# Performance work log

Measured on AMD Instinct MI355X. Metric: run time of the kernel, lower is better.

## Reference

```python
import jax, jax.numpy as jnp
import numpy as np

NEG_INF = -9e15
ALPHA = 0.2  # LeakyReLU negative slope used by GraphAttentionLayer


def gat_layer(h, adj, W, a, concat):
    # h: [N, din], W: [din, dout], a: [2*dout, 1]
    Wh = h @ W                              # [N, dout]
    dout = W.shape[1]
    f1 = Wh @ a[:dout]                      # [N, 1]
    f2 = Wh @ a[dout:]                      # [N, 1]
    e = jax.nn.leaky_relu(f1 + f2.T, negative_slope=ALPHA)   # [N, N]
    att = jax.nn.softmax(jnp.where(adj > 0, e, NEG_INF), axis=1)
    hp = att @ Wh                           # [N, dout]
    out = jax.nn.elu(hp) if concat else hp
    return out, att


def setup_inputs() -> dict:
    key = jax.random.key(0)
    ks = jax.random.split(key, 6)
    N, d_in, d_hid, d_out = 8192, 256, 128, 64
    features = jax.random.normal(ks[0], (N, d_in), dtype=jnp.float32)
    adj = (jax.random.uniform(ks[1], (N, N)) < 0.01).astype(jnp.float32)
    s = 0.1
    W1 = jax.random.normal(ks[2], (d_in, d_hid), dtype=jnp.float32) * s
    a1 = jax.random.normal(ks[3], (2 * d_hid, 1), dtype=jnp.float32) * s
    W2 = jax.random.normal(ks[4], (d_hid, d_out), dtype=jnp.float32) * s
    a2 = jax.random.normal(ks[5], (2 * d_out, 1), dtype=jnp.float32) * s
    return {"features": features, "adj": adj, "W1": W1, "a1": a1, "W2": W2, "a2": a2}


def reference(features, adj, W1, a1, W2, a2):
    h1, attention = gat_layer(features, adj, W1, a1, concat=True)   # gat1 (elu)
    h2, _ = gat_layer(h1, adj, W2, a2, concat=False)                 # gat2
    row_mask = (adj.sum(axis=1) > 0).astype(h2.dtype)[:, None]       # [N, 1]
    genenet_res = jax.nn.sigmoid(h2 @ h2.T) * row_mask               # inner-product decoder
    return h2, genenet_res, attention
```

## Files before the change

kernel.cpp:

```cpp
#include <hip/hip_runtime.h>
#include <cstdint>
#include <cstddef>

#define NN 8192
#define DIN 256
#define DHID 128
#define DOUT 64
#define MAXDEG 256

using short8  = __attribute__((ext_vector_type(8))) short;
using floatx4 = __attribute__((ext_vector_type(4))) float;

__device__ inline unsigned short f2bf(float x) {
  union { float f; unsigned u; } c; c.f = x;
  unsigned r = (c.u + 0x7FFFu + ((c.u >> 16) & 1u)) >> 16;
  return (unsigned short)r;
}

__global__ __launch_bounds__(256) void k_gemm1(const float* __restrict__ feat,
                                               const float* __restrict__ W1,
                                               float* __restrict__ Wh1) {
  __shared__ float Ws[64 * DHID];
  __shared__ float Fs[64][65];
  const int tid = threadIdx.x;
  const int cx = tid & 31;
  const int ry = tid >> 5;
  const int r0 = blockIdx.x * 64;
  float acc[8][4] = {};
  for (int kc = 0; kc < DIN; kc += 64) {
    const float4* src = (const float4*)(W1 + (size_t)kc * DHID);
    float4* dst = (float4*)Ws;
    #pragma unroll
    for (int i = 0; i < 8; ++i) dst[i * 256 + tid] = src[i * 256 + tid];
    #pragma unroll
    for (int i = 0; i < 4; ++i) {
      int idx = i * 256 + tid;
      int row = idx >> 4, kq = idx & 15;
      float4 v = *(const float4*)(feat + (size_t)(r0 + row) * DIN + kc + kq * 4);
      Fs[row][kq * 4 + 0] = v.x; Fs[row][kq * 4 + 1] = v.y;
      Fs[row][kq * 4 + 2] = v.z; Fs[row][kq * 4 + 3] = v.w;
    }
    __syncthreads();
    #pragma unroll 4
    for (int k = 0; k < 64; ++k) {
      float4 w = *(const float4*)(Ws + k * DHID + cx * 4);
      #pragma unroll
      for (int r = 0; r < 8; ++r) {
        float f = Fs[ry * 8 + r][k];
        acc[r][0] += f * w.x; acc[r][1] += f * w.y;
        acc[r][2] += f * w.z; acc[r][3] += f * w.w;
      }
    }
    __syncthreads();
  }
  #pragma unroll
  for (int r = 0; r < 8; ++r) {
    float4 o = make_float4(acc[r][0], acc[r][1], acc[r][2], acc[r][3]);
    *(float4*)(Wh1 + (size_t)(r0 + ry * 8 + r) * DHID + cx * 4) = o;
  }
}

__global__ __launch_bounds__(256) void k_gemm2(const float* __restrict__ h1,
                                               const float* __restrict__ W2,
                                               float* __restrict__ Wh2) {
  __shared__ float Ws[64 * DOUT];
  __shared__ float Fs[128][65];
  const int tid = threadIdx.x;
  const int cx = tid & 15;
  const int ry = tid >> 4;
  const int r0 = blockIdx.x * 128;
  float acc[8][4] = {};
  for (int kc = 0; kc < DHID; kc += 64) {
    const float4* src = (const float4*)(W2 + (size_t)kc * DOUT);
    float4* dst = (float4*)Ws;
    #pragma unroll
    for (int i = 0; i < 4; ++i) dst[i * 256 + tid] = src[i * 256 + tid];
    #pragma unroll
    for (int i = 0; i < 8; ++i) {
      int idx = i * 256 + tid;
      int row = idx >> 4, kq = idx & 15;
      float4 v = *(const float4*)(h1 + (size_t)(r0 + row) * DHID + kc + kq * 4);
      Fs[row][kq * 4 + 0] = v.x; Fs[row][kq * 4 + 1] = v.y;
      Fs[row][kq * 4 + 2] = v.z; Fs[row][kq * 4 + 3] = v.w;
    }
    __syncthreads();
    #pragma unroll 4
    for (int k = 0; k < 64; ++k) {
      float4 w = *(const float4*)(Ws + k * DOUT + cx * 4);
      #pragma unroll
      for (int r = 0; r < 8; ++r) {
        float f = Fs[ry * 8 + r][k];
        acc[r][0] += f * w.x; acc[r][1] += f * w.y;
        acc[r][2] += f * w.z; acc[r][3] += f * w.w;
      }
    }
    __syncthreads();
  }
  #pragma unroll
  for (int r = 0; r < 8; ++r) {
    float4 o = make_float4(acc[r][0], acc[r][1], acc[r][2], acc[r][3]);
    *(float4*)(Wh2 + (size_t)(r0 + ry * 8 + r) * DOUT + cx * 4) = o;
  }
}

__global__ __launch_bounds__(256) void k_fvec1(const float* __restrict__ Wh1,
                                               const float* __restrict__ a1,
                                               float* __restrict__ f1, float* __restrict__ f2) {
  int wv = threadIdx.x >> 6, lane = threadIdx.x & 63;
  int row = blockIdx.x * 4 + wv;
  float2 x = *(const float2*)(Wh1 + (size_t)row * DHID + lane * 2);
  float2 u = *(const float2*)(a1 + lane * 2);
  float2 v = *(const float2*)(a1 + DHID + lane * 2);
  float s1 = x.x * u.x + x.y * u.y;
  float s2 = x.x * v.x + x.y * v.y;
  #pragma unroll
  for (int off = 32; off; off >>= 1) { s1 += __shfl_down(s1, off); s2 += __shfl_down(s2, off); }
  if (lane == 0) { f1[row] = s1; f2[row] = s2; }
}

__global__ __launch_bounds__(256) void k_fvec2(const float* __restrict__ Wh2,
                                               const float* __restrict__ a2,
                                               float* __restrict__ f1, float* __restrict__ f2) {
  int wv = threadIdx.x >> 6, lane = threadIdx.x & 63;
  int row = blockIdx.x * 4 + wv;
  float x = Wh2[(size_t)row * DOUT + lane];
  float s1 = x * a2[lane];
  float s2 = x * a2[DOUT + lane];
  #pragma unroll
  for (int off = 32; off; off >>= 1) { s1 += __shfl_down(s1, off); s2 += __shfl_down(s2, off); }
  if (lane == 0) { f1[row] = s1; f2[row] = s2; }
}

__global__ __launch_bounds__(256) void k_att1(const float* __restrict__ adj,
                                              const float* __restrict__ f1,
                                              const float* __restrict__ f2,
                                              const float* __restrict__ Wh1,
                                              float* __restrict__ att_out,
                                              float* __restrict__ h1,
                                              int* __restrict__ csr,
                                              int* __restrict__ degree) {
  __shared__ int   scols[MAXDEG];
  __shared__ float sval[MAXDEG];
  __shared__ float red[256];
  __shared__ int   cnt;
  const int tid = threadIdx.x;
  const int row = blockIdx.x;
  if (tid == 0) cnt = 0;
  __syncthreads();
  const float4* arow = (const float4*)(adj + (size_t)row * NN);
  #pragma unroll
  for (int it = 0; it < 8; ++it) {
    int idx = it * 256 + tid;
    float4 v = arow[idx];
    if (v.x > 0.0f) { int s = atomicAdd(&cnt, 1); if (s < MAXDEG) scols[s] = idx * 4 + 0; }
    if (v.y > 0.0f) { int s = atomicAdd(&cnt, 1); if (s < MAXDEG) scols[s] = idx * 4 + 1; }
    if (v.z > 0.0f) { int s = atomicAdd(&cnt, 1); if (s < MAXDEG) scols[s] = idx * 4 + 2; }
    if (v.w > 0.0f) { int s = atomicAdd(&cnt, 1); if (s < MAXDEG) scols[s] = idx * 4 + 3; }
  }
  __syncthreads();
  const int deg = min(cnt, MAXDEG);
  if (tid == 0) degree[row] = deg;
  for (int t = tid; t < deg; t += 256) csr[(size_t)row * MAXDEG + t] = scols[t];
  const float base = f1[row];
  float lmax = -3.0e38f;
  for (int t = tid; t < deg; t += 256) {
    float e = base + f2[scols[t]];
    e = e > 0.0f ? e : 0.2f * e;
    sval[t] = e;
    lmax = fmaxf(lmax, e);
  }
  red[tid] = lmax; __syncthreads();
  #pragma unroll
  for (int off = 128; off; off >>= 1) { if (tid < off) red[tid] = fmaxf(red[tid], red[tid + off]); __syncthreads(); }
  const float m = red[0];
  __syncthreads();
  float lsum = 0.0f;
  for (int t = tid; t < deg; t += 256) { float ex = expf(sval[t] - m); sval[t] = ex; lsum += ex; }
  red[tid] = lsum; __syncthreads();
  #pragma unroll
  for (int off = 128; off; off >>= 1) { if (tid < off) red[tid] += red[tid + off]; __syncthreads(); }
  const float inv = 1.0f / red[0];
  __syncthreads();
  for (int t = tid; t < deg; t += 256) sval[t] *= inv;
  const float fill = (deg == 0) ? (1.0f / (float)NN) : 0.0f;
  float4 fv = make_float4(fill, fill, fill, fill);
  float4* orow = (float4*)(att_out + (size_t)row * NN);
  #pragma unroll
  for (int it = 0; it < 8; ++it) orow[it * 256 + tid] = fv;
  __syncthreads();
  for (int t = tid; t < deg; t += 256) att_out[(size_t)row * NN + scols[t]] = sval[t];
  const int d = tid & 127, g = tid >> 7;
  float acc = 0.0f;
  if (deg > 0) {
    for (int t = g; t < deg; t += 2) acc += sval[t] * Wh1[(size_t)scols[t] * DHID + d];
  } else {
    for (int r = g; r < NN; r += 2) acc += Wh1[(size_t)r * DHID + d];
    acc *= (1.0f / (float)NN);
  }
  __syncthreads();
  red[tid] = acc; __syncthreads();
  if (tid < 128) {
    float h = red[tid] + red[tid + 128];
    h = h > 0.0f ? h : (expf(h) - 1.0f);
    h1[(size_t)row * DHID + tid] = h;
  }
}

__global__ __launch_bounds__(256) void k_att2(const int* __restrict__ csr,
                                              const int* __restrict__ degree,
                                              const float* __restrict__ f1,
                                              const float* __restrict__ f2,
                                              const float* __restrict__ Wh2,
                                              float* __restrict__ h2) {
  __shared__ int   scols[MAXDEG];
  __shared__ float sval[MAXDEG];
  __shared__ float red[256];
  const int tid = threadIdx.x;
  const int row = blockIdx.x;
  const int deg = degree[row];
  for (int t = tid; t < deg; t += 256) scols[t] = csr[(size_t)row * MAXDEG + t];
  __syncthreads();
  const float base = f1[row];
  float lmax = -3.0e38f;
  for (int t = tid; t < deg; t += 256) {
    float e = base + f2[scols[t]];
    e = e > 0.0f ? e : 0.2f * e;
    sval[t] = e;
    lmax = fmaxf(lmax, e);
  }
  red[tid] = lmax; __syncthreads();
  #pragma unroll
  for (int off = 128; off; off >>= 1) { if (tid < off) red[tid] = fmaxf(red[tid], red[tid + off]); __syncthreads(); }
  const float m = red[0];
  __syncthreads();
  float lsum = 0.0f;
  for (int t = tid; t < deg; t += 256) { float ex = expf(sval[t] - m); sval[t] = ex; lsum += ex; }
  red[tid] = lsum; __syncthreads();
  #pragma unroll
  for (int off = 128; off; off >>= 1) { if (tid < off) red[tid] += red[tid + off]; __syncthreads(); }
  const float inv = 1.0f / red[0];
  __syncthreads();
  for (int t = tid; t < deg; t += 256) sval[t] *= inv;
  __syncthreads();
  const int d = tid & 63, g = tid >> 6;
  float acc = 0.0f;
  if (deg > 0) {
    for (int t = g; t < deg; t += 4) acc += sval[t] * Wh2[(size_t)scols[t] * DOUT + d];
  } else {
    for (int r = g; r < NN; r += 4) acc += Wh2[(size_t)r * DOUT + d];
    acc *= (1.0f / (float)NN);
  }
  red[tid] = acc; __syncthreads();
  if (tid < 64) h2[(size_t)row * DOUT + tid] = red[tid] + red[tid + 64] + red[tid + 128] + red[tid + 192];
}

__global__ __launch_bounds__(256) void k_genenet(const float* __restrict__ h2,
                                                 const int* __restrict__ degree,
                                                 float* __restrict__ out) {
  __shared__ unsigned short As[128 * 72];
  __shared__ unsigned short Bs[128 * 72];
  __shared__ float dmask[128];
  const int tid = threadIdx.x;
  const int R0 = blockIdx.x * 128, C0 = blockIdx.y * 128;
  #pragma unroll
  for (int it = 0; it < 8; ++it) {
    int idx = it * 256 + tid;
    int r = idx >> 4, kq = idx & 15;
    float4 va = *(const float4*)(h2 + (size_t)(R0 + r) * DOUT + kq * 4);
    float4 vb = *(const float4*)(h2 + (size_t)(C0 + r) * DOUT + kq * 4);
    ushort4 ba, bb;
    ba.x = f2bf(va.x); ba.y = f2bf(va.y); ba.z = f2bf(va.z); ba.w = f2bf(va.w);
    bb.x = f2bf(vb.x); bb.y = f2bf(vb.y); bb.z = f2bf(vb.z); bb.w = f2bf(vb.w);
    *(ushort4*)&As[r * 72 + kq * 4] = ba;
    *(ushort4*)&Bs[r * 72 + kq * 4] = bb;
  }
  if (tid < 128) dmask[tid] = (degree[R0 + tid] > 0) ? 1.0f : 0.0f;
  __syncthreads();
  const int wave = tid >> 6, lane = tid & 63;
  const int wr = wave >> 1, wc = wave & 1;
  const int lr = lane & 15, quad = lane >> 4;
  short8 a[4][2], b[4][2];
  #pragma unroll
  for (int mi = 0; mi < 4; ++mi) {
    int r = wr * 64 + mi * 16 + lr;
    a[mi][0] = *(const short8*)(const void*)&As[r * 72 + quad * 8];
    a[mi][1] = *(const short8*)(const void*)&As[r * 72 + quad * 8 + 32];
  }
  #pragma unroll
  for (int ni = 0; ni < 4; ++ni) {
    int r = wc * 64 + ni * 16 + lr;
    b[ni][0] = *(const short8*)(const void*)&Bs[r * 72 + quad * 8];
    b[ni][1] = *(const short8*)(const void*)&Bs[r * 72 + quad * 8 + 32];
  }
  floatx4 acc[4][4] = {};
  #pragma unroll
  for (int mi = 0; mi < 4; ++mi)
    #pragma unroll
    for (int ni = 0; ni < 4; ++ni) {
      acc[mi][ni] = __builtin_amdgcn_mfma_f32_16x16x32_bf16(a[mi][0], b[ni][0], acc[mi][ni], 0, 0, 0);
      acc[mi][ni] = __builtin_amdgcn_mfma_f32_16x16x32_bf16(a[mi][1], b[ni][1], acc[mi][ni], 0, 0, 0);
    }
  #pragma unroll
  for (int mi = 0; mi < 4; ++mi) {
    #pragma unroll
    for (int reg = 0; reg < 4; ++reg) {
      int lrow = wr * 64 + mi * 16 + quad * 4 + reg;
      float msk = dmask[lrow];
      size_t rowoff = (size_t)(R0 + lrow) * NN + C0 + wc * 64;
      #pragma unroll
      for (int ni = 0; ni < 4; ++ni) {
        float x = acc[mi][ni][reg];
        float s = 1.0f / (1.0f + __expf(-x));
        out[rowoff + ni * 16 + lr] = s * msk;
      }
    }
  }
}

extern "C" void kernel_launch(void* const* d_in, const int* in_sizes, int n_in,
                              void* d_out, int out_size, void* d_ws, size_t ws_size,
                              hipStream_t stream) {
  const float* feat = (const float*)d_in[0];
  const float* adj  = (const float*)d_in[1];
  const float* W1   = (const float*)d_in[2];
  const float* a1   = (const float*)d_in[3];
  const float* W2   = (const float*)d_in[4];
  const float* a2   = (const float*)d_in[5];
  float* out = (float*)d_out;
  float* h2_out  = out;
  float* gen_out = out + (size_t)NN * DOUT;
  float* att_out = gen_out + (size_t)NN * NN;
  int*   csr  = (int*)gen_out;
  float* Wh1  = gen_out + 2097152;
  float* h1   = gen_out + 3145728;
  float* Wh2  = gen_out + 4194304;
  float* f1_1 = gen_out + 4718592;
  float* f2_1 = f1_1 + NN;
  float* f1_2 = f2_1 + NN;
  float* f2_2 = f1_2 + NN;
  int* degree = (int*)d_ws;

  k_gemm1  <<<dim3(NN / 64),  dim3(256), 0, stream>>>(feat, W1, Wh1);
  k_fvec1  <<<dim3(NN / 4),   dim3(256), 0, stream>>>(Wh1, a1, f1_1, f2_1);
  k_att1   <<<dim3(NN),       dim3(256), 0, stream>>>(adj, f1_1, f2_1, Wh1, att_out, h1, csr, degree);
  k_gemm2  <<<dim3(NN / 128), dim3(256), 0, stream>>>(h1, W2, Wh2);
  k_fvec2  <<<dim3(NN / 4),   dim3(256), 0, stream>>>(Wh2, a2, f1_2, f2_2);
  k_att2   <<<dim3(NN),       dim3(256), 0, stream>>>(csr, degree, f1_2, f2_2, Wh2, h2_out);
  k_genenet<<<dim3(64, 64),   dim3(256), 0, stream>>>(h2_out, degree, gen_out);
}
```

Before: 845.5 us.

## Use wave-shuffle softmax, float2 aggregation, swizzled LDS and fast reciprocal

Both attention kernels replace the strided softmax loops and tree reductions in shared memory with one-element-per-thread wave shuffles, assuming the degree is at most 256. They also use fast __expf. The att1 kernel issues all adjacency loads up front and aggregates Wh1 with float2 loads across four groups. The genenet kernel swaps padded LDS tiles for an XOR-style swizzle and uses hardware rcp in the sigmoid. Together these cut barriers and LDS traffic, at a small cost in precision.

```diff
diff --git a/kernel.cpp b/kernel.cpp
--- a/kernel.cpp
+++ b/kernel.cpp
@@ -132,133 +132,148 @@
 }
 
 __global__ __launch_bounds__(256) void k_att1(const float* __restrict__ adj,
-                                              const float* __restrict__ f1,
-                                              const float* __restrict__ f2,
+                                              const float* __restrict__ f1v,
+                                              const float* __restrict__ f2v,
                                               const float* __restrict__ Wh1,
                                               float* __restrict__ att_out,
                                               float* __restrict__ h1,
                                               int* __restrict__ csr,
                                               int* __restrict__ degree) {
-  __shared__ int   scols[MAXDEG];
-  __shared__ float sval[MAXDEG];
-  __shared__ float red[256];
-  __shared__ int   cnt;
+  __shared__ int    scols[MAXDEG];
+  __shared__ float  sval[MAXDEG];
+  __shared__ float  xred[8];
+  __shared__ float2 red2[256];
+  __shared__ int    cnt;
   const int tid = threadIdx.x;
   const int row = blockIdx.x;
+  const int wv = tid >> 6, lane = tid & 63;
   if (tid == 0) cnt = 0;
   __syncthreads();
   const float4* arow = (const float4*)(adj + (size_t)row * NN);
+  float4 v[8];
+  #pragma unroll
+  for (int it = 0; it < 8; ++it) v[it] = arow[it * 256 + tid];
   #pragma unroll
   for (int it = 0; it < 8; ++it) {
-    int idx = it * 256 + tid;
-    float4 v = arow[idx];
-    if (v.x > 0.0f) { int s = atomicAdd(&cnt, 1); if (s < MAXDEG) scols[s] = idx * 4 + 0; }
-    if (v.y > 0.0f) { int s = atomicAdd(&cnt, 1); if (s < MAXDEG) scols[s] = idx * 4 + 1; }
-    if (v.z > 0.0f) { int s = atomicAdd(&cnt, 1); if (s < MAXDEG) scols[s] = idx * 4 + 2; }
-    if (v.w > 0.0f) { int s = atomicAdd(&cnt, 1); if (s < MAXDEG) scols[s] = idx * 4 + 3; }
+    int base4 = (it * 256 + tid) * 4;
+    if (v[it].x > 0.0f) { int s = atomicAdd(&cnt, 1); if (s < MAXDEG) scols[s] = base4; }
+    if (v[it].y > 0.0f) { int s = atomicAdd(&cnt, 1); if (s < MAXDEG) scols[s] = base4 + 1; }
+    if (v[it].z > 0.0f) { int s = atomicAdd(&cnt, 1); if (s < MAXDEG) scols[s] = base4 + 2; }
+    if (v[it].w > 0.0f) { int s = atomicAdd(&cnt, 1); if (s < MAXDEG) scols[s] = base4 + 3; }
   }
   __syncthreads();
   const int deg = min(cnt, MAXDEG);
   if (tid == 0) degree[row] = deg;
-  for (int t = tid; t < deg; t += 256) csr[(size_t)row * MAXDEG + t] = scols[t];
-  const float base = f1[row];
-  float lmax = -3.0e38f;
-  for (int t = tid; t < deg; t += 256) {
-    float e = base + f2[scols[t]];
-    e = e > 0.0f ? e : 0.2f * e;
-    sval[t] = e;
-    lmax = fmaxf(lmax, e);
-  }
-  red[tid] = lmax; __syncthreads();
-  #pragma unroll
-  for (int off = 128; off; off >>= 1) { if (tid < off) red[tid] = fmaxf(red[tid], red[tid + off]); __syncthreads(); }
-  const float m = red[0];
-  __syncthreads();
-  float lsum = 0.0f;
-  for (int t = tid; t < deg; t += 256) { float ex = expf(sval[t] - m); sval[t] = ex; lsum += ex; }
-  red[tid] = lsum; __syncthreads();
-  #pragma unroll
-  for (int off = 128; off; off >>= 1) { if (tid < off) red[tid] += red[tid + off]; __syncthreads(); }
-  const float inv = 1.0f / red[0];
-  __syncthreads();
-  for (int t = tid; t < deg; t += 256) sval[t] *= inv;
+  int col = -1; float e = -3.0e38f;
+  if (tid < deg) {
+    col = scols[tid];
+    csr[(size_t)row * MAXDEG + tid] = col;
+    float t = f1v[row] + f2v[col];
+    e = t > 0.0f ? t : 0.2f * t;
+  }
+  float m = e;
+  #pragma unroll
+  for (int off = 32; off; off >>= 1) m = fmaxf(m, __shfl_xor(m, off));
+  if (lane == 0) xred[wv] = m;
+  __syncthreads();
+  m = fmaxf(fmaxf(xred[0], xred[1]), fmaxf(xred[2], xred[3]));
+  float ex = (tid < deg) ? __expf(e - m) : 0.0f;
+  float sm = ex;
+  #pragma unroll
+  for (int off = 32; off; off >>= 1) sm += __shfl_xor(sm, off);
+  if (lane == 0) xred[4 + wv] = sm;
+  __syncthreads();
+  const float inv = 1.0f / (xred[4] + xred[5] + xred[6] + xred[7]);
+  const float p = ex * inv;
+  if (tid < deg) sval[tid] = p;
   const float fill = (deg == 0) ? (1.0f / (float)NN) : 0.0f;
   float4 fv = make_float4(fill, fill, fill, fill);
   float4* orow = (float4*)(att_out + (size_t)row * NN);
   #pragma unroll
   for (int it = 0; it < 8; ++it) orow[it * 256 + tid] = fv;
   __syncthreads();
-  for (int t = tid; t < deg; t += 256) att_out[(size_t)row * NN + scols[t]] = sval[t];
-  const int d = tid & 127, g = tid >> 7;
-  float acc = 0.0f;
+  if (tid < deg) att_out[(size_t)row * NN + col] = p;
+  const int g = tid >> 6;
+  float2 acc = make_float2(0.0f, 0.0f);
   if (deg > 0) {
-    for (int t = g; t < deg; t += 2) acc += sval[t] * Wh1[(size_t)scols[t] * DHID + d];
+    for (int t = g; t < deg; t += 4) {
+      float sv = sval[t];
+      float2 w = *(const float2*)(Wh1 + (size_t)scols[t] * DHID + lane * 2);
+      acc.x += sv * w.x; acc.y += sv * w.y;
+    }
   } else {
-    for (int r = g; r < NN; r += 2) acc += Wh1[(size_t)r * DHID + d];
-    acc *= (1.0f / (float)NN);
-  }
-  __syncthreads();
-  red[tid] = acc; __syncthreads();
-  if (tid < 128) {
-    float h = red[tid] + red[tid + 128];
-    h = h > 0.0f ? h : (expf(h) - 1.0f);
-    h1[(size_t)row * DHID + tid] = h;
+    for (int r = g; r < NN; r += 4) {
+      float2 w = *(const float2*)(Wh1 + (size_t)r * DHID + lane * 2);
+      acc.x += w.x; acc.y += w.y;
+    }
+    acc.x *= (1.0f / (float)NN); acc.y *= (1.0f / (float)NN);
+  }
+  red2[tid] = acc;
+  __syncthreads();
+  if (tid < 64) {
+    float2 a0 = red2[tid], a1 = red2[tid + 64], a2 = red2[tid + 128], a3 = red2[tid + 192];
+    float hx = a0.x + a1.x + a2.x + a3.x;
+    float hy = a0.y + a1.y + a2.y + a3.y;
+    hx = hx > 0.0f ? hx : (__expf(hx) - 1.0f);
+    hy = hy > 0.0f ? hy : (__expf(hy) - 1.0f);
+    *(float2*)(h1 + (size_t)row * DHID + tid * 2) = make_float2(hx, hy);
   }
 }
 
 __global__ __launch_bounds__(256) void k_att2(const int* __restrict__ csr,
                                               const int* __restrict__ degree,
-                                              const float* __restrict__ f1,
-                                              const float* __restrict__ f2,
+                                              const float* __restrict__ f1v,
+                                              const float* __restrict__ f2v,
                                               const float* __restrict__ Wh2,
                                               float* __restrict__ h2) {
   __shared__ int   scols[MAXDEG];
   __shared__ float sval[MAXDEG];
+  __shared__ float xred[8];
   __shared__ float red[256];
   const int tid = threadIdx.x;
   const int row = blockIdx.x;
+  const int wv = tid >> 6, lane = tid & 63;
   const int deg = degree[row];
-  for (int t = tid; t < deg; t += 256) scols[t] = csr[(size_t)row * MAXDEG + t];
-  __syncthreads();
-  const float base = f1[row];
-  float lmax = -3.0e38f;
-  for (int t = tid; t < deg; t += 256) {
-    float e = base + f2[scols[t]];
-    e = e > 0.0f ? e : 0.2f * e;
-    sval[t] = e;
-    lmax = fmaxf(lmax, e);
-  }
-  red[tid] = lmax; __syncthreads();
-  #pragma unroll
-  for (int off = 128; off; off >>= 1) { if (tid < off) red[tid] = fmaxf(red[tid], red[tid + off]); __syncthreads(); }
-  const float m = red[0];
-  __syncthreads();
-  float lsum = 0.0f;
-  for (int t = tid; t < deg; t += 256) { float ex = expf(sval[t] - m); sval[t] = ex; lsum += ex; }
-  red[tid] = lsum; __syncthreads();
-  #pragma unroll
-  for (int off = 128; off; off >>= 1) { if (tid < off) red[tid] += red[tid + off]; __syncthreads(); }
-  const float inv = 1.0f / red[0];
-  __syncthreads();
-  for (int t = tid; t < deg; t += 256) sval[t] *= inv;
-  __syncthreads();
-  const int d = tid & 63, g = tid >> 6;
+  int col = -1; float e = -3.0e38f;
+  if (tid < deg) {
+    col = csr[(size_t)row * MAXDEG + tid];
+    scols[tid] = col;
+    float t = f1v[row] + f2v[col];
+    e = t > 0.0f ? t : 0.2f * t;
+  }
+  float m = e;
+  #pragma unroll
+  for (int off = 32; off; off >>= 1) m = fmaxf(m, __shfl_xor(m, off));
+  if (lane == 0) xred[wv] = m;
+  __syncthreads();
+  m = fmaxf(fmaxf(xred[0], xred[1]), fmaxf(xred[2], xred[3]));
+  float ex = (tid < deg) ? __expf(e - m) : 0.0f;
+  float sm = ex;
+  #pragma unroll
+  for (int off = 32; off; off >>= 1) sm += __shfl_xor(sm, off);
+  if (lane == 0) xred[4 + wv] = sm;
+  __syncthreads();
+  const float inv = 1.0f / (xred[4] + xred[5] + xred[6] + xred[7]);
+  if (tid < deg) sval[tid] = ex * inv;
+  __syncthreads();
+  const int g = tid >> 6;
   float acc = 0.0f;
   if (deg > 0) {
-    for (int t = g; t < deg; t += 4) acc += sval[t] * Wh2[(size_t)scols[t] * DOUT + d];
+    for (int t = g; t < deg; t += 4) acc += sval[t] * Wh2[(size_t)scols[t] * DOUT + lane];
   } else {
-    for (int r = g; r < NN; r += 4) acc += Wh2[(size_t)r * DOUT + d];
+    for (int r = g; r < NN; r += 4) acc += Wh2[(size_t)r * DOUT + lane];
     acc *= (1.0f / (float)NN);
   }
-  red[tid] = acc; __syncthreads();
+  red[tid] = acc;
+  __syncthreads();
   if (tid < 64) h2[(size_t)row * DOUT + tid] = red[tid] + red[tid + 64] + red[tid + 128] + red[tid + 192];
 }
 
 __global__ __launch_bounds__(256) void k_genenet(const float* __restrict__ h2,
                                                  const int* __restrict__ degree,
                                                  float* __restrict__ out) {
-  __shared__ unsigned short As[128 * 72];
-  __shared__ unsigned short Bs[128 * 72];
+  __shared__ unsigned short As[128 * 64];
+  __shared__ unsigned short Bs[128 * 64];
   __shared__ float dmask[128];
   const int tid = threadIdx.x;
   const int R0 = blockIdx.x * 128, C0 = blockIdx.y * 128;
@@ -266,13 +281,14 @@
   for (int it = 0; it < 8; ++it) {
     int idx = it * 256 + tid;
     int r = idx >> 4, kq = idx & 15;
+    int c = kq >> 1, hf = kq & 1;
+    int off = r * 64 + (((c + r) & 7) << 3) + (hf << 2);
     float4 va = *(const float4*)(h2 + (size_t)(R0 + r) * DOUT + kq * 4);
     float4 vb = *(const float4*)(h2 + (size_t)(C0 + r) * DOUT + kq * 4);
-    ushort4 ba, bb;
-    ba.x = f2bf(va.x); ba.y = f2bf(va.y); ba.z = f2bf(va.z); ba.w = f2bf(va.w);
-    bb.x = f2bf(vb.x); bb.y = f2bf(vb.y); bb.z = f2bf(vb.z); bb.w = f2bf(vb.w);
-    *(ushort4*)&As[r * 72 + kq * 4] = ba;
-    *(ushort4*)&Bs[r * 72 + kq * 4] = bb;
+    ushort4 ba = make_ushort4(f2bf(va.x), f2bf(va.y), f2bf(va.z), f2bf(va.w));
+    ushort4 bb = make_ushort4(f2bf(vb.x), f2bf(vb.y), f2bf(vb.z), f2bf(vb.w));
+    *(ushort4*)&As[off] = ba;
+    *(ushort4*)&Bs[off] = bb;
   }
   if (tid < 128) dmask[tid] = (degree[R0 + tid] > 0) ? 1.0f : 0.0f;
   __syncthreads();
@@ -283,14 +299,20 @@
   #pragma unroll
   for (int mi = 0; mi < 4; ++mi) {
     int r = wr * 64 + mi * 16 + lr;
-    a[mi][0] = *(const short8*)(const void*)&As[r * 72 + quad * 8];
-    a[mi][1] = *(const short8*)(const void*)&As[r * 72 + quad * 8 + 32];
+    #pragma unroll
+    for (int j = 0; j < 2; ++j) {
+      int c = quad + 4 * j;
+      a[mi][j] = *(const short8*)(const void*)&As[r * 64 + (((c + r) & 7) << 3)];
+    }
   }
   #pragma unroll
   for (int ni = 0; ni < 4; ++ni) {
     int r = wc * 64 + ni * 16 + lr;
-    b[ni][0] = *(const short8*)(const void*)&Bs[r * 72 + quad * 8];
-    b[ni][1] = *(const short8*)(const void*)&Bs[r * 72 + quad * 8 + 32];
+    #pragma unroll
+    for (int j = 0; j < 2; ++j) {
+      int c = quad + 4 * j;
+      b[ni][j] = *(const short8*)(const void*)&Bs[r * 64 + (((c + r) & 7) << 3)];
+    }
   }
   floatx4 acc[4][4] = {};
   #pragma unroll
@@ -310,7 +332,7 @@
       #pragma unroll
       for (int ni = 0; ni < 4; ++ni) {
         float x = acc[mi][ni][reg];
-        float s = 1.0f / (1.0f + __expf(-x));
+        float s = __builtin_amdgcn_rcpf(1.0f + __expf(-x));
         out[rowoff + ni * 16 + lr] = s * msk;
       }
     }
```

Measured after the change: 800.7 us. 1.06x faster.
